# Kernel tuning notes

Hardware: AMD Instinct MI355X
Metric: run time of the kernel (lower is better)

Reference implementation:

```python
import jax, jax.numpy as jnp
import numpy as np

N_LAYERS = 2
N_ENT = 50000


def setup_inputs() -> dict:
    key = jax.random.key(0)
    k1, k2, k3, k4, k5 = jax.random.split(key, 5)
    R, N, D, E = 16, N_ENT, 128, 50000
    return {
        "ent_emb": jax.random.normal(k1, (N, D), dtype=jnp.float32),
        "rel_trans": jax.random.normal(k2, (R, D, D), dtype=jnp.float32) * (1.0 / np.sqrt(D)),
        "edge_val": jax.random.uniform(k3, (R, E), dtype=jnp.float32),
        "edge_row": jax.random.randint(k4, (R, E), 0, N, dtype=jnp.int32),
        "edge_col": jax.random.randint(k5, (R, E), 0, N, dtype=jnp.int32),
    }


def _spmm(row, col, val, emb):
    # out[i] = sum_{edges e with row[e]==i} val[e] * emb[col[e]]  (A @ emb)
    msgs = emb[col] * val[:, None]            # [E, d]
    return jax.ops.segment_sum(msgs, row, num_segments=N_ENT)  # [N, d]


def reference(ent_emb, rel_trans, edge_val, edge_row, edge_col):
    emb = ent_emb
    for _ in range(N_LAYERS):
        # per-relation sparse A_r @ emb -> [R, N, d]
        emb_acc = jax.vmap(_spmm, in_axes=(0, 0, 0, None))(edge_row, edge_col, edge_val, emb)
        # batched relation transform: rel_trans[r] @ emb_acc[r].T, transposed back
        tmp = jnp.einsum("rij,rnj->rni", rel_trans, emb_acc)  # [R, N, d]
        emb = jax.nn.relu(jnp.sum(tmp, axis=0))               # [N, d]
    # F.normalize: L2 along dim=1 with eps=1e-12
    norm = jnp.linalg.norm(emb, axis=1, keepdims=True)
    emb = emb / jnp.maximum(norm, 1e-12)
    return emb
```

## Files before the change

### kernel.cpp

```cpp
#include <hip/hip_runtime.h>
#include <stdint.h>

#define NE 50000
#define DD 128
#define RR 16
#define EE 50000
#define NT 64
#define NTOT (RR * NE)
#define SCAN_BLK 4096
#define NSCAN ((NTOT + SCAN_BLK - 1) / SCAN_BLK)

typedef short  shortx8 __attribute__((ext_vector_type(8)));
typedef short  shortx4 __attribute__((ext_vector_type(4)));
typedef float  floatx4 __attribute__((ext_vector_type(4)));

__device__ __forceinline__ unsigned short f2bf(float f) {
    unsigned u = __float_as_uint(f);
    u += 0x7fffu + ((u >> 16) & 1u);
    return (unsigned short)(u >> 16);
}
__device__ __forceinline__ float bf2f(unsigned short h) {
    return __uint_as_float(((unsigned)h) << 16);
}

#define ZB 782
#define TB 128
#define EB 6250
__global__ void prep_k(const float* __restrict__ rt, unsigned short* __restrict__ Tf,
                       const float4* __restrict__ emb, shortx4* __restrict__ embA,
                       int* __restrict__ counts) {
    int b = blockIdx.x, t = threadIdx.x;
    if (b < ZB) {
        int i4 = b * 256 + t;
        if (i4 < NTOT / 4) *(int4*)(counts + i4 * 4) = make_int4(0, 0, 0, 0);
    } else if (b < ZB + TB) {
        int c = (b - ZB) * 256 + t;
        int r = c >> 11, row = (c >> 4) & 127, cb = c & 15;
        int kt = cb >> 2, qq = cb & 3, rg = row >> 4, m = row & 15;
        const float4* src = (const float4*)(rt + (size_t)c * 8);
        float4 v0 = src[0], v1 = src[1];
        shortx8 w;
        w[0] = (short)f2bf(v0.x); w[1] = (short)f2bf(v0.y);
        w[2] = (short)f2bf(v0.z); w[3] = (short)f2bf(v0.w);
        w[4] = (short)f2bf(v1.x); w[5] = (short)f2bf(v1.y);
        w[6] = (short)f2bf(v1.z); w[7] = (short)f2bf(v1.w);
        size_t idx = ((((size_t)r * 8 + rg) * 4 + kt) * 64 + qq * 16 + m) * 8;
        *(shortx8*)(Tf + idx) = w;
    } else {
        int i = (b - ZB - TB) * 256 + t;
        if (i < NE * DD / 4) {
            float4 v = emb[i];
            shortx4 w;
            w[0] = (short)f2bf(v.x); w[1] = (short)f2bf(v.y);
            w[2] = (short)f2bf(v.z); w[3] = (short)f2bf(v.w);
            embA[i] = w;
        }
    }
}

__global__ void hist_k(const int* __restrict__ erow, int* __restrict__ counts,
                       uchar4* __restrict__ rank) {
    int r  = blockIdx.y;
    int i4 = blockIdx.x * 256 + threadIdx.x;
    if (i4 < EE / 4) {
        int4 rw = *(const int4*)(erow + (size_t)r * EE + i4 * 4);
        uchar4 rk;
        rk.x = (unsigned char)atomicAdd(&counts[rw.x * RR + r], 1);
        rk.y = (unsigned char)atomicAdd(&counts[rw.y * RR + r], 1);
        rk.z = (unsigned char)atomicAdd(&counts[rw.z * RR + r], 1);
        rk.w = (unsigned char)atomicAdd(&counts[rw.w * RR + r], 1);
        rank[(size_t)r * (EE / 4) + i4] = rk;
    }
}

__global__ void scanA(const int* __restrict__ c, int* __restrict__ bsum) {
    int b = blockIdx.x, t = threadIdx.x;
    int base = b * SCAN_BLK + t * 16;
    int s = 0;
    #pragma unroll
    for (int i = 0; i < 16; i++) {
        int idx = base + i;
        if (idx < NTOT) s += c[idx];
    }
    __shared__ int sh[256];
    sh[t] = s;
    __syncthreads();
    for (int off = 128; off > 0; off >>= 1) {
        if (t < off) sh[t] += sh[t + off];
        __syncthreads();
    }
    if (t == 0) bsum[b] = sh[0];
}

__global__ void scanC(const int* __restrict__ counts, int* __restrict__ rp,
                      const int* __restrict__ bsum) {
    int b = blockIdx.x, t = threadIdx.x;
    __shared__ int shb[256];
    shb[t] = (t < NSCAN) ? bsum[t] : 0;
    __syncthreads();
    for (int off = 1; off < 256; off <<= 1) {
        int add = (t >= off) ? shb[t - off] : 0;
        __syncthreads();
        shb[t] += add;
        __syncthreads();
    }
    int blockPrefix = (b > 0) ? shb[b - 1] : 0;
    int base = b * SCAN_BLK + t * 16;
    int vals[16];
    int s = 0;
    #pragma unroll
    for (int i = 0; i < 16; i++) {
        int idx = base + i;
        vals[i] = (idx < NTOT) ? counts[idx] : 0;
        s += vals[i];
    }
    __shared__ int sh[256];
    sh[t] = s;
    __syncthreads();
    for (int off = 1; off < 256; off <<= 1) {
        int add = (t >= off) ? sh[t - off] : 0;
        __syncthreads();
        sh[t] += add;
        __syncthreads();
    }
    int run = blockPrefix + sh[t] - s;
    #pragma unroll
    for (int i = 0; i < 16; i++) {
        int idx = base + i;
        if (idx < NTOT) {
            rp[idx] = run;
            run += vals[i];
            if (idx == NTOT - 1) rp[NTOT] = run;
        }
    }
}

__global__ void fill_k(const int* __restrict__ erow, const int* __restrict__ ecol,
                       const float* __restrict__ eval, const int* __restrict__ rp,
                       const uchar4* __restrict__ rank, int2* __restrict__ edges) {
    int r  = blockIdx.y;
    int i4 = blockIdx.x * 256 + threadIdx.x;
    if (i4 < EE / 4) {
        int4   rw = *(const int4*)(erow + (size_t)r * EE + i4 * 4);
        int4   cl = *(const int4*)(ecol + (size_t)r * EE + i4 * 4);
        float4 vl = *(const float4*)(eval + (size_t)r * EE + i4 * 4);
        uchar4 rk = rank[(size_t)r * (EE / 4) + i4];
        edges[rp[rw.x * RR + r] + rk.x] = make_int2(cl.x, __float_as_int(vl.x));
        edges[rp[rw.y * RR + r] + rk.y] = make_int2(cl.y, __float_as_int(vl.y));
        edges[rp[rw.z * RR + r] + rk.z] = make_int2(cl.z, __float_as_int(vl.z));
        edges[rp[rw.w * RR + r] + rk.w] = make_int2(cl.w, __float_as_int(vl.w));
    }
}

__device__ __forceinline__ void accum_chunks(float a0[8], float a1[8], float v,
                                             shortx8 c0, shortx8 c1) {
    #pragma unroll
    for (int j = 0; j < 8; j++) {
        a0[j] = fmaf(v, bf2f((unsigned short)c0[j]), a0[j]);
        a1[j] = fmaf(v, bf2f((unsigned short)c1[j]), a1[j]);
    }
}

template<bool FINAL>
__global__ __launch_bounds__(256, 4)
void layer_k(const unsigned short* __restrict__ embIn,
             const unsigned short* __restrict__ Tf,
             const int* __restrict__ rp,
             const int2* __restrict__ eg,
             unsigned short* __restrict__ embOut,
             float* __restrict__ outF)
{
    __shared__ __align__(16) unsigned short Bt[64 * 128];
    __shared__ float ssred[4][64];

    const int t    = threadIdx.x;
    const int lane = t & 63;
    const int w    = t >> 6;
    const int colq = lane & 15;
    const int q    = lane >> 4;
    const int n0   = blockIdx.x * NT;
    const int nsub = t >> 3;
    const int dgrp = t & 7;

    floatx4 acc[2][4];
    #pragma unroll
    for (int a = 0; a < 2; a++)
        #pragma unroll
        for (int c = 0; c < 4; c++)
            acc[a][c] = (floatx4){0.f, 0.f, 0.f, 0.f};

    #pragma unroll 1
    for (int r = 0; r < RR; r++) {
        int s_[2], c_[2];
        #pragma unroll
        for (int p = 0; p < 2; p++) {
            int n = n0 + p * 32 + nsub;
            bool ok = n < NE;
            int key = (ok ? n : 0) * RR + r;
            int a = rp[key], b2 = rp[key + 1];
            s_[p] = a; c_[p] = ok ? (b2 - a) : 0;
        }
        int   col0[2], col1[2];
        float v0_[2], v1_[2];
        #pragma unroll
        for (int p = 0; p < 2; p++) {
            int2 E0 = eg[s_[p]];
            int2 E1 = eg[s_[p] + 1];
            col0[p] = c_[p] > 0 ? E0.x : 0;
            col1[p] = c_[p] > 1 ? E1.x : 0;
            v0_[p]  = c_[p] > 0 ? __int_as_float(E0.y) : 0.f;
            v1_[p]  = c_[p] > 1 ? __int_as_float(E1.y) : 0.f;
        }
        shortx8 m[2][2][2];
        #pragma unroll
        for (int p = 0; p < 2; p++) {
            const unsigned short* r0 = embIn + (size_t)col0[p] * DD + dgrp * 8;
            const unsigned short* r1 = embIn + (size_t)col1[p] * DD + dgrp * 8;
            m[p][0][0] = *(const shortx8*)r0;
            m[p][0][1] = *(const shortx8*)(r0 + 64);
            m[p][1][0] = *(const shortx8*)r1;
            m[p][1][1] = *(const shortx8*)(r1 + 64);
        }
        #pragma unroll
        for (int p = 0; p < 2; p++) {
            float a0[8], a1[8];
            #pragma unroll
            for (int j = 0; j < 8; j++) { a0[j] = 0.f; a1[j] = 0.f; }
            accum_chunks(a0, a1, v0_[p], m[p][0][0], m[p][0][1]);
            accum_chunks(a0, a1, v1_[p], m[p][1][0], m[p][1][1]);
            if (c_[p] > 2) {
                #pragma unroll 1
                for (int k = s_[p] + 2; k < s_[p] + c_[p]; k++) {
                    int2 E = eg[k];
                    float v = __int_as_float(E.y);
                    const unsigned short* rw_ = embIn + (size_t)E.x * DD + dgrp * 8;
                    accum_chunks(a0, a1, v, *(const shortx8*)rw_, *(const shortx8*)(rw_ + 64));
                }
            }
            int nl = p * 32 + nsub;
            shortx8 w0, w1;
            #pragma unroll
            for (int j = 0; j < 8; j++) { w0[j] = (short)f2bf(a0[j]); w1[j] = (short)f2bf(a1[j]); }
            int pc = (dgrp ^ nl) & 7;
            *(shortx8*)&Bt[nl * 128 + pc * 8] = w0;
            *(shortx8*)&Bt[nl * 128 + (8 | pc) * 8] = w1;
        }
        __syncthreads();

        shortx8 afN[2];
        #pragma unroll
        for (int it2 = 0; it2 < 2; it2++)
            afN[it2] = *(const shortx8*)(Tf + ((((size_t)r * 8 + (w * 2 + it2)) * 4 + 0) * 64 + lane) * 8);
        #pragma unroll 1
        for (int kt = 0; kt < 4; kt++) {
            shortx8 afC[2];
            afC[0] = afN[0]; afC[1] = afN[1];
            if (kt < 3) {
                #pragma unroll
                for (int it2 = 0; it2 < 2; it2++)
                    afN[it2] = *(const shortx8*)(Tf + ((((size_t)r * 8 + (w * 2 + it2)) * 4 + (kt + 1)) * 64 + lane) * 8);
            }
            int lc = kt * 4 + q;
            shortx8 bfr[4];
            #pragma unroll
            for (int c = 0; c < 4; c++) {
                int nl = c * 16 + colq;
                int pc = (lc & 8) | ((lc ^ nl) & 7);
                bfr[c] = *(const shortx8*)&Bt[nl * 128 + pc * 8];
            }
            #pragma unroll
            for (int it2 = 0; it2 < 2; it2++)
                #pragma unroll
                for (int c = 0; c < 4; c++)
                    acc[it2][c] = __builtin_amdgcn_mfma_f32_16x16x32_bf16(afC[it2], bfr[c], acc[it2][c], 0, 0, 0);
        }
        __syncthreads();
    }

    if (!FINAL) {
        #pragma unroll
        for (int c = 0; c < 4; c++) {
            int n = n0 + c * 16 + colq;
            if (n < NE) {
                #pragma unroll
                for (int it2 = 0; it2 < 2; it2++) {
                    shortx4 wv;
                    #pragma unroll
                    for (int g = 0; g < 4; g++) {
                        float v = acc[it2][c][g];
                        v = v > 0.f ? v : 0.f;
                        wv[g] = (short)f2bf(v);
                    }
                    *(shortx4*)(embOut + ((size_t)n * DD + w * 32 + it2 * 16 + q * 4)) = wv;
                }
            }
        }
    } else {
        #pragma unroll
        for (int c = 0; c < 4; c++) {
            float ss = 0.f;
            #pragma unroll
            for (int it2 = 0; it2 < 2; it2++)
                #pragma unroll
                for (int g = 0; g < 4; g++) {
                    float v = acc[it2][c][g];
                    v = v > 0.f ? v : 0.f;
                    acc[it2][c][g] = v;
                    ss += v * v;
                }
            ss += __shfl_xor(ss, 16, 64);
            ss += __shfl_xor(ss, 32, 64);
            if (q == 0) ssred[w][c * 16 + colq] = ss;
        }
        __syncthreads();
        #pragma unroll
        for (int c = 0; c < 4; c++) {
            int nl = c * 16 + colq;
            float tot = ssred[0][nl] + ssred[1][nl] + ssred[2][nl] + ssred[3][nl];
            float scale = 1.f / fmaxf(sqrtf(tot), 1e-12f);
            int n = n0 + nl;
            if (n < NE) {
                #pragma unroll
                for (int it2 = 0; it2 < 2; it2++) {
                    floatx4 v4;
                    #pragma unroll
                    for (int g = 0; g < 4; g++) v4[g] = acc[it2][c][g] * scale;
                    *(floatx4*)(outF + ((size_t)n * DD + w * 32 + it2 * 16 + q * 4)) = v4;
                }
            }
        }
    }
}

static inline size_t align256(size_t x) { return (x + 255) & ~(size_t)255; }

extern "C" void kernel_launch(void* const* d_in, const int* in_sizes, int n_in,
                              void* d_out, int out_size, void* d_ws, size_t ws_size,
                              hipStream_t stream)
{
    const float* ent_emb   = (const float*)d_in[0];
    const float* rel_trans = (const float*)d_in[1];
    const float* edge_val  = (const float*)d_in[2];
    const int*   edge_row  = (const int*)d_in[3];
    const int*   edge_col  = (const int*)d_in[4];
    float* out = (float*)d_out;

    char* ws = (char*)d_ws;
    size_t off = 0;
    int* counts = (int*)(ws + off);  off = align256(off + (size_t)NTOT * 4);
    int* rpf    = (int*)(ws + off);  off = align256(off + ((size_t)NTOT + 1) * 4);
    int* bsum   = (int*)(ws + off);  off = align256(off + 256 * 4);
    uchar4* rank = (uchar4*)(ws + off); off = align256(off + (size_t)NTOT);
    int2* edges = (int2*)(ws + off); off = align256(off + ((size_t)NTOT + 4) * 8);
    unsigned short* Tf   = (unsigned short*)(ws + off); off = align256(off + (size_t)RR * DD * DD * 2);
    unsigned short* embA = (unsigned short*)(ws + off); off = align256(off + (size_t)NE * DD * 2);
    unsigned short* embB = (unsigned short*)(ws + off); off = align256(off + (size_t)NE * DD * 2);

    prep_k<<<ZB + TB + EB, 256, 0, stream>>>(rel_trans, Tf, (const float4*)ent_emb,
                                             (shortx4*)embA, counts);
    dim3 eg_grid((EE / 4 + 255) / 256, RR);
    hist_k<<<eg_grid, 256, 0, stream>>>(edge_row, counts, rank);
    scanA<<<NSCAN, 256, 0, stream>>>(counts, bsum);
    scanC<<<NSCAN, 256, 0, stream>>>(counts, rpf, bsum);
    fill_k<<<eg_grid, 256, 0, stream>>>(edge_row, edge_col, edge_val, rpf, rank, edges);

    int nb = (NE + NT - 1) / NT;
    layer_k<false><<<nb, 256, 0, stream>>>(embA, Tf, rpf, edges, embB, nullptr);
    layer_k<true ><<<nb, 256, 0, stream>>>(embB, Tf, rpf, edges, nullptr, out);
}
```

Baseline: 328.9 us.

## Stage per-block CSR and edges in LDS, prefetch next relation gather, fuse histogram

Each layer block now loads its slice of row pointers and up to 2048 edges into shared memory once, then issues the next relation's first embedding gathers right after the barrier so they overlap the MFMA transform of the current relation. The histogram kernel is merged into the prep kernel and the zeroing of counts is replaced by a memset. In exchange, shared memory use grows and launch bounds drop to 3 waves per SIMD, lowering occupancy, and the prefetched gather registers add register pressure.

```diff
diff --git a/kernel.cpp b/kernel.cpp
--- a/kernel.cpp
+++ b/kernel.cpp
@@ -9,6 +9,7 @@
 #define NTOT (RR * NE)
 #define SCAN_BLK 4096
 #define NSCAN ((NTOT + SCAN_BLK - 1) / SCAN_BLK)
+#define EDCAP 2048
 
 typedef short  shortx8 __attribute__((ext_vector_type(8)));
 typedef short  shortx4 __attribute__((ext_vector_type(4)));
@@ -23,18 +24,16 @@
     return __uint_as_float(((unsigned)h) << 16);
 }
 
-#define ZB 782
 #define TB 128
 #define EB 6250
+#define HB 782
 __global__ void prep_k(const float* __restrict__ rt, unsigned short* __restrict__ Tf,
                        const float4* __restrict__ emb, shortx4* __restrict__ embA,
-                       int* __restrict__ counts) {
+                       const int* __restrict__ erow, int* __restrict__ counts,
+                       uchar4* __restrict__ rank) {
     int b = blockIdx.x, t = threadIdx.x;
-    if (b < ZB) {
-        int i4 = b * 256 + t;
-        if (i4 < NTOT / 4) *(int4*)(counts + i4 * 4) = make_int4(0, 0, 0, 0);
-    } else if (b < ZB + TB) {
-        int c = (b - ZB) * 256 + t;
+    if (b < TB) {
+        int c = b * 256 + t;
         int r = c >> 11, row = (c >> 4) & 127, cb = c & 15;
         int kt = cb >> 2, qq = cb & 3, rg = row >> 4, m = row & 15;
         const float4* src = (const float4*)(rt + (size_t)c * 8);
@@ -46,8 +45,8 @@
         w[6] = (short)f2bf(v1.z); w[7] = (short)f2bf(v1.w);
         size_t idx = ((((size_t)r * 8 + rg) * 4 + kt) * 64 + qq * 16 + m) * 8;
         *(shortx8*)(Tf + idx) = w;
-    } else {
-        int i = (b - ZB - TB) * 256 + t;
+    } else if (b < TB + EB) {
+        int i = (b - TB) * 256 + t;
         if (i < NE * DD / 4) {
             float4 v = emb[i];
             shortx4 w;
@@ -55,21 +54,19 @@
             w[2] = (short)f2bf(v.z); w[3] = (short)f2bf(v.w);
             embA[i] = w;
         }
-    }
-}
-
-__global__ void hist_k(const int* __restrict__ erow, int* __restrict__ counts,
-                       uchar4* __restrict__ rank) {
-    int r  = blockIdx.y;
-    int i4 = blockIdx.x * 256 + threadIdx.x;
-    if (i4 < EE / 4) {
-        int4 rw = *(const int4*)(erow + (size_t)r * EE + i4 * 4);
-        uchar4 rk;
-        rk.x = (unsigned char)atomicAdd(&counts[rw.x * RR + r], 1);
-        rk.y = (unsigned char)atomicAdd(&counts[rw.y * RR + r], 1);
-        rk.z = (unsigned char)atomicAdd(&counts[rw.z * RR + r], 1);
-        rk.w = (unsigned char)atomicAdd(&counts[rw.w * RR + r], 1);
-        rank[(size_t)r * (EE / 4) + i4] = rk;
+    } else {
+        int e4 = (b - TB - EB) * 256 + t;
+        if (e4 < RR * EE / 4) {
+            int r  = e4 / (EE / 4);
+            int i4 = e4 - r * (EE / 4);
+            int4 rw = *(const int4*)(erow + (size_t)r * EE + i4 * 4);
+            uchar4 rk;
+            rk.x = (unsigned char)atomicAdd(&counts[rw.x * RR + r], 1);
+            rk.y = (unsigned char)atomicAdd(&counts[rw.y * RR + r], 1);
+            rk.z = (unsigned char)atomicAdd(&counts[rw.z * RR + r], 1);
+            rk.w = (unsigned char)atomicAdd(&counts[rw.w * RR + r], 1);
+            rank[(size_t)r * (EE / 4) + i4] = rk;
+        }
     }
 }
 
@@ -162,7 +159,7 @@
 }
 
 template<bool FINAL>
-__global__ __launch_bounds__(256, 4)
+__global__ __launch_bounds__(256, 3)
 void layer_k(const unsigned short* __restrict__ embIn,
              const unsigned short* __restrict__ Tf,
              const int* __restrict__ rp,
@@ -171,6 +168,8 @@
              float* __restrict__ outF)
 {
     __shared__ __align__(16) unsigned short Bt[64 * 128];
+    __shared__ int  rpL[NT * RR + 1];
+    __shared__ int2 edL[EDCAP];
     __shared__ float ssred[4][64];
 
     const int t    = threadIdx.x;
@@ -181,6 +180,29 @@
     const int n0   = blockIdx.x * NT;
     const int nsub = t >> 3;
     const int dgrp = t & 7;
+    const int base = n0 * RR;
+
+    const int sBase = rp[base];
+    const int sEnd  = rp[(base + NT * RR < NTOT) ? base + NT * RR : NTOT];
+    #pragma unroll
+    for (int i = 0; i < 5; i++) {
+        int idx = i * 256 + t;
+        if (idx <= NT * RR) {
+            int gi = base + idx;
+            rpL[idx] = rp[gi < NTOT ? gi : NTOT];
+        }
+    }
+    {
+        int cnt = sEnd - sBase;
+        if (cnt > EDCAP) cnt = EDCAP;
+        for (int i = t; i < cnt; i += 256) edL[i] = eg[sBase + i];
+    }
+    __syncthreads();
+
+    auto getE = [&](int idx) -> int2 {
+        int o = idx - sBase;
+        return (o < EDCAP) ? edL[o] : eg[idx];
+    };
 
     floatx4 acc[2][4];
     #pragma unroll
@@ -189,49 +211,47 @@
         for (int c = 0; c < 4; c++)
             acc[a][c] = (floatx4){0.f, 0.f, 0.f, 0.f};
 
-    #pragma unroll 1
-    for (int r = 0; r < RR; r++) {
-        int s_[2], c_[2];
+    int   sC[2], cC[2];
+    float v0C[2], v1C[2];
+    shortx8 m[2][2][2];
+
+    auto issueGather = [&](int r) {
         #pragma unroll
         for (int p = 0; p < 2; p++) {
-            int n = n0 + p * 32 + nsub;
-            bool ok = n < NE;
-            int key = (ok ? n : 0) * RR + r;
-            int a = rp[key], b2 = rp[key + 1];
-            s_[p] = a; c_[p] = ok ? (b2 - a) : 0;
-        }
-        int   col0[2], col1[2];
-        float v0_[2], v1_[2];
-        #pragma unroll
-        for (int p = 0; p < 2; p++) {
-            int2 E0 = eg[s_[p]];
-            int2 E1 = eg[s_[p] + 1];
-            col0[p] = c_[p] > 0 ? E0.x : 0;
-            col1[p] = c_[p] > 1 ? E1.x : 0;
-            v0_[p]  = c_[p] > 0 ? __int_as_float(E0.y) : 0.f;
-            v1_[p]  = c_[p] > 1 ? __int_as_float(E1.y) : 0.f;
-        }
-        shortx8 m[2][2][2];
-        #pragma unroll
-        for (int p = 0; p < 2; p++) {
-            const unsigned short* r0 = embIn + (size_t)col0[p] * DD + dgrp * 8;
-            const unsigned short* r1 = embIn + (size_t)col1[p] * DD + dgrp * 8;
+            int li = (p * 32 + nsub) * RR + r;
+            int s = rpL[li], e = rpL[li + 1];
+            int c = e - s;
+            int2 E0 = getE(s);
+            int2 E1 = getE(s + 1);
+            int col0 = c > 0 ? E0.x : 0;
+            int col1 = c > 1 ? E1.x : 0;
+            v0C[p] = c > 0 ? __int_as_float(E0.y) : 0.f;
+            v1C[p] = c > 1 ? __int_as_float(E1.y) : 0.f;
+            sC[p] = s; cC[p] = c;
+            const unsigned short* r0 = embIn + (size_t)col0 * DD + dgrp * 8;
+            const unsigned short* r1 = embIn + (size_t)col1 * DD + dgrp * 8;
             m[p][0][0] = *(const shortx8*)r0;
             m[p][0][1] = *(const shortx8*)(r0 + 64);
             m[p][1][0] = *(const shortx8*)r1;
             m[p][1][1] = *(const shortx8*)(r1 + 64);
         }
+    };
+
+    issueGather(0);
+
+    #pragma unroll 1
+    for (int r = 0; r < RR; r++) {
         #pragma unroll
         for (int p = 0; p < 2; p++) {
             float a0[8], a1[8];
             #pragma unroll
             for (int j = 0; j < 8; j++) { a0[j] = 0.f; a1[j] = 0.f; }
-            accum_chunks(a0, a1, v0_[p], m[p][0][0], m[p][0][1]);
-            accum_chunks(a0, a1, v1_[p], m[p][1][0], m[p][1][1]);
-            if (c_[p] > 2) {
+            accum_chunks(a0, a1, v0C[p], m[p][0][0], m[p][0][1]);
+            accum_chunks(a0, a1, v1C[p], m[p][1][0], m[p][1][1]);
+            if (cC[p] > 2) {
                 #pragma unroll 1
-                for (int k = s_[p] + 2; k < s_[p] + c_[p]; k++) {
-                    int2 E = eg[k];
+                for (int k = sC[p] + 2; k < sC[p] + cC[p]; k++) {
+                    int2 E = getE(k);
                     float v = __int_as_float(E.y);
                     const unsigned short* rw_ = embIn + (size_t)E.x * DD + dgrp * 8;
                     accum_chunks(a0, a1, v, *(const shortx8*)rw_, *(const shortx8*)(rw_ + 64));
@@ -246,6 +266,8 @@
             *(shortx8*)&Bt[nl * 128 + (8 | pc) * 8] = w1;
         }
         __syncthreads();
+
+        if (r + 1 < RR) issueGather(r + 1);
 
         shortx8 afN[2];
         #pragma unroll
@@ -351,17 +373,17 @@
     int* rpf    = (int*)(ws + off);  off = align256(off + ((size_t)NTOT + 1) * 4);
     int* bsum   = (int*)(ws + off);  off = align256(off + 256 * 4);
     uchar4* rank = (uchar4*)(ws + off); off = align256(off + (size_t)NTOT);
-    int2* edges = (int2*)(ws + off); off = align256(off + ((size_t)NTOT + 4) * 8);
+    int2* edges = (int2*)(ws + off); off = align256(off + ((size_t)NTOT + 8) * 8);
     unsigned short* Tf   = (unsigned short*)(ws + off); off = align256(off + (size_t)RR * DD * DD * 2);
     unsigned short* embA = (unsigned short*)(ws + off); off = align256(off + (size_t)NE * DD * 2);
     unsigned short* embB = (unsigned short*)(ws + off); off = align256(off + (size_t)NE * DD * 2);
 
-    prep_k<<<ZB + TB + EB, 256, 0, stream>>>(rel_trans, Tf, (const float4*)ent_emb,
-                                             (shortx4*)embA, counts);
-    dim3 eg_grid((EE / 4 + 255) / 256, RR);
-    hist_k<<<eg_grid, 256, 0, stream>>>(edge_row, counts, rank);
+    hipMemsetAsync(counts, 0, (size_t)NTOT * 4, stream);
+    prep_k<<<TB + EB + HB, 256, 0, stream>>>(rel_trans, Tf, (const float4*)ent_emb,
+                                             (shortx4*)embA, edge_row, counts, rank);
     scanA<<<NSCAN, 256, 0, stream>>>(counts, bsum);
     scanC<<<NSCAN, 256, 0, stream>>>(counts, rpf, bsum);
+    dim3 eg_grid((EE / 4 + 255) / 256, RR);
     fill_k<<<eg_grid, 256, 0, stream>>>(edge_row, edge_col, edge_val, rpf, rank, edges);
 
     int nb = (NE + NT - 1) / NT;
```

Result: slower. 381.2 us (+15.9%).

## Replace CSR build with fixed-capacity per-row buckets plus overflow list

Applied to the files above, without the earlier changes.

Replaces the histogram, two-pass scan and fill kernels with one bucket-fill pass: each (node, relation) key gets a fixed 8-slot bucket filled by atomic rank, and any excess goes to a global overflow list. The fill is folded into the prep kernel, and zeroing moves to a single memset. The layer kernel reads buckets directly, always gathers four embedding rows (zero-valued slots hit row 0), and prefetches the next relation's bucket and rows across the sync. The cost is a much larger zeroed workspace (about 51 MB of buckets), extra wasted gathers for empty slots, lower occupancy bounds, and a linear overflow scan per key whenever overflow occurs.

```diff
diff --git a/kernel.cpp b/kernel.cpp
--- a/kernel.cpp
+++ b/kernel.cpp
@@ -7,8 +7,8 @@
 #define EE 50000
 #define NT 64
 #define NTOT (RR * NE)
-#define SCAN_BLK 4096
-#define NSCAN ((NTOT + SCAN_BLK - 1) / SCAN_BLK)
+#define CAP 8
+#define OVCAP 65536
 
 typedef short  shortx8 __attribute__((ext_vector_type(8)));
 typedef short  shortx4 __attribute__((ext_vector_type(4)));
@@ -23,18 +23,18 @@
     return __uint_as_float(((unsigned)h) << 16);
 }
 
-#define ZB 782
 #define TB 128
 #define EB 6250
+#define FB 782
 __global__ void prep_k(const float* __restrict__ rt, unsigned short* __restrict__ Tf,
                        const float4* __restrict__ emb, shortx4* __restrict__ embA,
-                       int* __restrict__ counts) {
+                       const int* __restrict__ erow, const int* __restrict__ ecol,
+                       const float* __restrict__ eval,
+                       int* __restrict__ counts, int* __restrict__ ovfh,
+                       int4* __restrict__ ovf, int2* __restrict__ edges) {
     int b = blockIdx.x, t = threadIdx.x;
-    if (b < ZB) {
-        int i4 = b * 256 + t;
-        if (i4 < NTOT / 4) *(int4*)(counts + i4 * 4) = make_int4(0, 0, 0, 0);
-    } else if (b < ZB + TB) {
-        int c = (b - ZB) * 256 + t;
+    if (b < TB) {
+        int c = b * 256 + t;
         int r = c >> 11, row = (c >> 4) & 127, cb = c & 15;
         int kt = cb >> 2, qq = cb & 3, rg = row >> 4, m = row & 15;
         const float4* src = (const float4*)(rt + (size_t)c * 8);
@@ -46,8 +46,8 @@
         w[6] = (short)f2bf(v1.z); w[7] = (short)f2bf(v1.w);
         size_t idx = ((((size_t)r * 8 + rg) * 4 + kt) * 64 + qq * 16 + m) * 8;
         *(shortx8*)(Tf + idx) = w;
-    } else {
-        int i = (b - ZB - TB) * 256 + t;
+    } else if (b < TB + EB) {
+        int i = (b - TB) * 256 + t;
         if (i < NE * DD / 4) {
             float4 v = emb[i];
             shortx4 w;
@@ -55,100 +55,29 @@
             w[2] = (short)f2bf(v.z); w[3] = (short)f2bf(v.w);
             embA[i] = w;
         }
-    }
-}
-
-__global__ void hist_k(const int* __restrict__ erow, int* __restrict__ counts,
-                       uchar4* __restrict__ rank) {
-    int r  = blockIdx.y;
-    int i4 = blockIdx.x * 256 + threadIdx.x;
-    if (i4 < EE / 4) {
-        int4 rw = *(const int4*)(erow + (size_t)r * EE + i4 * 4);
-        uchar4 rk;
-        rk.x = (unsigned char)atomicAdd(&counts[rw.x * RR + r], 1);
-        rk.y = (unsigned char)atomicAdd(&counts[rw.y * RR + r], 1);
-        rk.z = (unsigned char)atomicAdd(&counts[rw.z * RR + r], 1);
-        rk.w = (unsigned char)atomicAdd(&counts[rw.w * RR + r], 1);
-        rank[(size_t)r * (EE / 4) + i4] = rk;
-    }
-}
-
-__global__ void scanA(const int* __restrict__ c, int* __restrict__ bsum) {
-    int b = blockIdx.x, t = threadIdx.x;
-    int base = b * SCAN_BLK + t * 16;
-    int s = 0;
-    #pragma unroll
-    for (int i = 0; i < 16; i++) {
-        int idx = base + i;
-        if (idx < NTOT) s += c[idx];
-    }
-    __shared__ int sh[256];
-    sh[t] = s;
-    __syncthreads();
-    for (int off = 128; off > 0; off >>= 1) {
-        if (t < off) sh[t] += sh[t + off];
-        __syncthreads();
-    }
-    if (t == 0) bsum[b] = sh[0];
-}
-
-__global__ void scanC(const int* __restrict__ counts, int* __restrict__ rp,
-                      const int* __restrict__ bsum) {
-    int b = blockIdx.x, t = threadIdx.x;
-    __shared__ int shb[256];
-    shb[t] = (t < NSCAN) ? bsum[t] : 0;
-    __syncthreads();
-    for (int off = 1; off < 256; off <<= 1) {
-        int add = (t >= off) ? shb[t - off] : 0;
-        __syncthreads();
-        shb[t] += add;
-        __syncthreads();
-    }
-    int blockPrefix = (b > 0) ? shb[b - 1] : 0;
-    int base = b * SCAN_BLK + t * 16;
-    int vals[16];
-    int s = 0;
-    #pragma unroll
-    for (int i = 0; i < 16; i++) {
-        int idx = base + i;
-        vals[i] = (idx < NTOT) ? counts[idx] : 0;
-        s += vals[i];
-    }
-    __shared__ int sh[256];
-    sh[t] = s;
-    __syncthreads();
-    for (int off = 1; off < 256; off <<= 1) {
-        int add = (t >= off) ? sh[t - off] : 0;
-        __syncthreads();
-        sh[t] += add;
-        __syncthreads();
-    }
-    int run = blockPrefix + sh[t] - s;
-    #pragma unroll
-    for (int i = 0; i < 16; i++) {
-        int idx = base + i;
-        if (idx < NTOT) {
-            rp[idx] = run;
-            run += vals[i];
-            if (idx == NTOT - 1) rp[NTOT] = run;
-        }
-    }
-}
-
-__global__ void fill_k(const int* __restrict__ erow, const int* __restrict__ ecol,
-                       const float* __restrict__ eval, const int* __restrict__ rp,
-                       const uchar4* __restrict__ rank, int2* __restrict__ edges) {
-    int r  = blockIdx.y;
-    int i4 = blockIdx.x * 256 + threadIdx.x;
-    if (i4 < EE / 4) {
-        int4   rw = *(const int4*)(erow + (size_t)r * EE + i4 * 4);
-        int4   cl = *(const int4*)(ecol + (size_t)r * EE + i4 * 4);
-        float4 vl = *(const float4*)(eval + (size_t)r * EE + i4 * 4);
-        uchar4 rk = rank[(size_t)r * (EE / 4) + i4];
-        edges[rp[rw.x * RR + r] + rk.x] = make_int2(cl.x, __float_as_int(vl.x));
-        edges[rp[rw.y * RR + r] + rk.y] = make_int2(cl.y, __float_as_int(vl.y));
-        edges[rp[rw.z * RR + r] + rk.z] = make_int2(cl.z, __float_as_int(vl.z));
-        edges[rp[rw.w * RR + r] + rk.w] = make_int2(cl.w, __float_as_int(vl.w));
+    } else {
+        int e4 = (b - TB - EB) * 256 + t;
+        if (e4 < RR * EE / 4) {
+            int r  = e4 / (EE / 4);
+            int i4 = e4 - r * (EE / 4);
+            int4   rw = *(const int4*)(erow + (size_t)r * EE + i4 * 4);
+            int4   cl = *(const int4*)(ecol + (size_t)r * EE + i4 * 4);
+            float4 vl = *(const float4*)(eval + (size_t)r * EE + i4 * 4);
+            int key, rk;
+            #define PUT(N_, C_, V_)                                             \
+                key = (N_) * RR + r;                                            \
+                rk  = atomicAdd(&counts[key], 1);                               \
+                if (rk < CAP) edges[(size_t)key * CAP + rk] =                   \
+                    make_int2((C_), __float_as_int(V_));                        \
+                else { int o = atomicAdd(ovfh, 1);                              \
+                       if (o < OVCAP) ovf[o] = make_int4(key, (C_),             \
+                                                __float_as_int(V_), 0); }
+            PUT(rw.x, cl.x, vl.x)
+            PUT(rw.y, cl.y, vl.y)
+            PUT(rw.z, cl.z, vl.z)
+            PUT(rw.w, cl.w, vl.w)
+            #undef PUT
+        }
     }
 }
 
@@ -162,11 +91,13 @@
 }
 
 template<bool FINAL>
-__global__ __launch_bounds__(256, 4)
+__global__ __launch_bounds__(256, 3)
 void layer_k(const unsigned short* __restrict__ embIn,
              const unsigned short* __restrict__ Tf,
-             const int* __restrict__ rp,
+             const int* __restrict__ counts,
              const int2* __restrict__ eg,
+             const int* __restrict__ ovfh,
+             const int4* __restrict__ ovf,
              unsigned short* __restrict__ embOut,
              float* __restrict__ outF)
 {
@@ -182,6 +113,14 @@
     const int nsub = t >> 3;
     const int dgrp = t & 7;
 
+    const int  nId[2] = { n0 + nsub, n0 + 32 + nsub };
+    const bool okp[2] = { nId[0] < NE, nId[1] < NE };
+    const int  kb[2]  = { (okp[0] ? nId[0] : 0) * RR, (okp[1] ? nId[1] : 0) * RR };
+
+    int ovfn = ovfh[0];
+    if (ovfn > OVCAP) ovfn = OVCAP;
+    if (ovfn < 0) ovfn = 0;
+
     floatx4 acc[2][4];
     #pragma unroll
     for (int a = 0; a < 2; a++)
@@ -189,52 +128,85 @@
         for (int c = 0; c < 4; c++)
             acc[a][c] = (floatx4){0.f, 0.f, 0.f, 0.f};
 
+    int4 eaC[2], ebC[2];
+    int  cntC[2];
+    shortx8 m[2][2][2];
+
+    #pragma unroll
+    for (int p = 0; p < 2; p++) {
+        const int4* bkt = (const int4*)(eg + (size_t)(kb[p] + 0) * CAP);
+        eaC[p] = bkt[0];
+        ebC[p] = bkt[1];
+        cntC[p] = counts[kb[p] + 0];
+    }
+    #pragma unroll
+    for (int p = 0; p < 2; p++) {
+        const unsigned short* r0 = embIn + (size_t)eaC[p].x * DD + dgrp * 8;
+        const unsigned short* r1 = embIn + (size_t)eaC[p].z * DD + dgrp * 8;
+        m[p][0][0] = *(const shortx8*)r0;
+        m[p][0][1] = *(const shortx8*)(r0 + 64);
+        m[p][1][0] = *(const shortx8*)r1;
+        m[p][1][1] = *(const shortx8*)(r1 + 64);
+    }
+
     #pragma unroll 1
     for (int r = 0; r < RR; r++) {
-        int s_[2], c_[2];
+        int4 eaN[2], ebN[2];
+        int  cntN[2];
+        if (r + 1 < RR) {
+            #pragma unroll
+            for (int p = 0; p < 2; p++) {
+                const int4* bkt = (const int4*)(eg + (size_t)(kb[p] + r + 1) * CAP);
+                eaN[p] = bkt[0];
+                ebN[p] = bkt[1];
+                cntN[p] = counts[kb[p] + r + 1];
+            }
+        }
+        shortx8 e23[2][2][2];
         #pragma unroll
         for (int p = 0; p < 2; p++) {
-            int n = n0 + p * 32 + nsub;
-            bool ok = n < NE;
-            int key = (ok ? n : 0) * RR + r;
-            int a = rp[key], b2 = rp[key + 1];
-            s_[p] = a; c_[p] = ok ? (b2 - a) : 0;
-        }
-        int   col0[2], col1[2];
-        float v0_[2], v1_[2];
-        #pragma unroll
-        for (int p = 0; p < 2; p++) {
-            int2 E0 = eg[s_[p]];
-            int2 E1 = eg[s_[p] + 1];
-            col0[p] = c_[p] > 0 ? E0.x : 0;
-            col1[p] = c_[p] > 1 ? E1.x : 0;
-            v0_[p]  = c_[p] > 0 ? __int_as_float(E0.y) : 0.f;
-            v1_[p]  = c_[p] > 1 ? __int_as_float(E1.y) : 0.f;
-        }
-        shortx8 m[2][2][2];
-        #pragma unroll
-        for (int p = 0; p < 2; p++) {
-            const unsigned short* r0 = embIn + (size_t)col0[p] * DD + dgrp * 8;
-            const unsigned short* r1 = embIn + (size_t)col1[p] * DD + dgrp * 8;
-            m[p][0][0] = *(const shortx8*)r0;
-            m[p][0][1] = *(const shortx8*)(r0 + 64);
-            m[p][1][0] = *(const shortx8*)r1;
-            m[p][1][1] = *(const shortx8*)(r1 + 64);
+            const unsigned short* r2 = embIn + (size_t)ebC[p].x * DD + dgrp * 8;
+            const unsigned short* r3 = embIn + (size_t)ebC[p].z * DD + dgrp * 8;
+            e23[p][0][0] = *(const shortx8*)r2;
+            e23[p][0][1] = *(const shortx8*)(r2 + 64);
+            e23[p][1][0] = *(const shortx8*)r3;
+            e23[p][1][1] = *(const shortx8*)(r3 + 64);
         }
         #pragma unroll
         for (int p = 0; p < 2; p++) {
             float a0[8], a1[8];
             #pragma unroll
             for (int j = 0; j < 8; j++) { a0[j] = 0.f; a1[j] = 0.f; }
-            accum_chunks(a0, a1, v0_[p], m[p][0][0], m[p][0][1]);
-            accum_chunks(a0, a1, v1_[p], m[p][1][0], m[p][1][1]);
-            if (c_[p] > 2) {
+            float v0 = okp[p] ? __int_as_float(eaC[p].y) : 0.f;
+            float v1 = okp[p] ? __int_as_float(eaC[p].w) : 0.f;
+            float v2 = okp[p] ? __int_as_float(ebC[p].y) : 0.f;
+            float v3 = okp[p] ? __int_as_float(ebC[p].w) : 0.f;
+            accum_chunks(a0, a1, v0, m[p][0][0], m[p][0][1]);
+            accum_chunks(a0, a1, v1, m[p][1][0], m[p][1][1]);
+            accum_chunks(a0, a1, v2, e23[p][0][0], e23[p][0][1]);
+            accum_chunks(a0, a1, v3, e23[p][1][0], e23[p][1][1]);
+            int cc = okp[p] ? cntC[p] : 0;
+            if (cc > 4) {
+                int ce = cc < CAP ? cc : CAP;
+                const int2* b2 = eg + (size_t)(kb[p] + r) * CAP;
                 #pragma unroll 1
-                for (int k = s_[p] + 2; k < s_[p] + c_[p]; k++) {
-                    int2 E = eg[k];
+                for (int k = 4; k < ce; k++) {
+                    int2 E = b2[k];
                     float v = __int_as_float(E.y);
                     const unsigned short* rw_ = embIn + (size_t)E.x * DD + dgrp * 8;
                     accum_chunks(a0, a1, v, *(const shortx8*)rw_, *(const shortx8*)(rw_ + 64));
+                }
+            }
+            if (ovfn) {
+                int myKey = okp[p] ? kb[p] + r : -1;
+                #pragma unroll 1
+                for (int i = 0; i < ovfn; i++) {
+                    int4 o = ovf[i];
+                    if (o.x == myKey) {
+                        float v = __int_as_float(o.z);
+                        const unsigned short* rw_ = embIn + (size_t)o.y * DD + dgrp * 8;
+                        accum_chunks(a0, a1, v, *(const shortx8*)rw_, *(const shortx8*)(rw_ + 64));
+                    }
                 }
             }
             int nl = p * 32 + nsub;
@@ -247,6 +219,18 @@
         }
         __syncthreads();
 
+        if (r + 1 < RR) {
+            #pragma unroll
+            for (int p = 0; p < 2; p++) {
+                const unsigned short* r0 = embIn + (size_t)eaN[p].x * DD + dgrp * 8;
+                const unsigned short* r1 = embIn + (size_t)eaN[p].z * DD + dgrp * 8;
+                m[p][0][0] = *(const shortx8*)r0;
+                m[p][0][1] = *(const shortx8*)(r0 + 64);
+                m[p][1][0] = *(const shortx8*)r1;
+                m[p][1][1] = *(const shortx8*)(r1 + 64);
+                eaC[p] = eaN[p]; ebC[p] = ebN[p]; cntC[p] = cntN[p];
+            }
+        }
         shortx8 afN[2];
         #pragma unroll
         for (int it2 = 0; it2 < 2; it2++)
@@ -347,24 +331,20 @@
 
     char* ws = (char*)d_ws;
     size_t off = 0;
-    int* counts = (int*)(ws + off);  off = align256(off + (size_t)NTOT * 4);
-    int* rpf    = (int*)(ws + off);  off = align256(off + ((size_t)NTOT + 1) * 4);
-    int* bsum   = (int*)(ws + off);  off = align256(off + 256 * 4);
-    uchar4* rank = (uchar4*)(ws + off); off = align256(off + (size_t)NTOT);
-    int2* edges = (int2*)(ws + off); off = align256(off + ((size_t)NTOT + 4) * 8);
+    int*  counts = (int*)(ws + off);  off = align256(off + (size_t)NTOT * 4);
+    int*  ovfh   = (int*)(ws + off);  off = align256(off + 256);
+    int4* ovf    = (int4*)(ws + off); off = align256(off + (size_t)OVCAP * 16);
+    int2* edges  = (int2*)(ws + off); off = align256(off + (size_t)NTOT * CAP * 8);
+    size_t zspan = off;
     unsigned short* Tf   = (unsigned short*)(ws + off); off = align256(off + (size_t)RR * DD * DD * 2);
     unsigned short* embA = (unsigned short*)(ws + off); off = align256(off + (size_t)NE * DD * 2);
     unsigned short* embB = (unsigned short*)(ws + off); off = align256(off + (size_t)NE * DD * 2);
 
-    prep_k<<<ZB + TB + EB, 256, 0, stream>>>(rel_trans, Tf, (const float4*)ent_emb,
-                                             (shortx4*)embA, counts);
-    dim3 eg_grid((EE / 4 + 255) / 256, RR);
-    hist_k<<<eg_grid, 256, 0, stream>>>(edge_row, counts, rank);
-    scanA<<<NSCAN, 256, 0, stream>>>(counts, bsum);
-    scanC<<<NSCAN, 256, 0, stream>>>(counts, rpf, bsum);
-    fill_k<<<eg_grid, 256, 0, stream>>>(edge_row, edge_col, edge_val, rpf, rank, edges);
-
+    hipMemsetAsync(ws, 0, zspan, stream);
+    prep_k<<<TB + EB + FB, 256, 0, stream>>>(rel_trans, Tf, (const float4*)ent_emb,
+                                             (shortx4*)embA, edge_row, edge_col, edge_val,
+                                             counts, ovfh, ovf, edges);
     int nb = (NE + NT - 1) / NT;
-    layer_k<false><<<nb, 256, 0, stream>>>(embA, Tf, rpf, edges, embB, nullptr);
-    layer_k<true ><<<nb, 256, 0, stream>>>(embB, Tf, rpf, edges, nullptr, out);
-}
+    layer_k<false><<<nb, 256, 0, stream>>>(embA, Tf, counts, edges, ovfh, ovf, embB, nullptr);
+    layer_k<true ><<<nb, 256, 0, stream>>>(embB, Tf, counts, edges, ovfh, ovf, nullptr, out);
+}
```

Result: slower. 516.0 us (+56.9%).
